# Kernel tuning notes

Hardware: AMD Instinct MI355X
Metric: run time of the kernel (lower is better)

## Reference

```python
import jax, jax.numpy as jnp
import numpy as np

B, N, DIM = 4, 2048, 1024
HEADS, DIM_HEAD = 16, 64
INNER = HEADS * DIM_HEAD


def setup_inputs() -> dict:
    key = jax.random.key(0)
    kx, kw = jax.random.split(key)
    x = jax.random.normal(kx, (B, N, DIM), dtype=jnp.float32)
    # Dense kernel [in_features, out_features], no bias
    w_qkv = jax.random.normal(kw, (DIM, 3 * INNER), dtype=jnp.float32) * (DIM ** -0.5)
    return {"x": x, "w_qkv": w_qkv}


def reference(x, w_qkv):
    scale = DIM_HEAD ** (-0.5)
    qkv = jnp.einsum('bnc,cf->bnf', x, w_qkv)  # [B, N, 3*INNER]
    q, k, v = jnp.split(qkv, 3, axis=-1)
    # 'b n (h d) -> b h n d'
    def to_heads(t):
        return t.reshape(B, N, HEADS, DIM_HEAD).transpose(0, 2, 1, 3)
    q, k, v = map(to_heads, (q, k, v))
    dots = jnp.einsum('bhid,bhjd->bhij', q, k) * scale  # [B, H, N, N]
    attn = jax.nn.softmax(dots, axis=-1)
    out = jnp.einsum('bhij,bhjd->bhid', attn, v)  # [B, H, N, D]
    # 'b h n d -> b n (h d)'
    return out.transpose(0, 2, 1, 3).reshape(B, N, INNER)
```

## Files before the change

kernel.cpp:

```cpp
#include <hip/hip_runtime.h>
#include <hip/hip_bf16.h>
#include <math.h>

typedef __bf16 bf16x2 __attribute__((ext_vector_type(2)));
typedef __bf16 bf16x4 __attribute__((ext_vector_type(4)));
typedef __bf16 bf16x8 __attribute__((ext_vector_type(8)));
typedef float f32x4 __attribute__((ext_vector_type(4)));
typedef float f32x16 __attribute__((ext_vector_type(16)));

#define MFMA16(a, b, c) __builtin_amdgcn_mfma_f32_16x16x32_bf16(a, b, c, 0, 0, 0)
#define MFMA32(a, b, c) __builtin_amdgcn_mfma_f32_32x32x16_bf16(a, b, c, 0, 0, 0)
#define QSCALE 0.1803368801111204f

__device__ __forceinline__ void gload_lds16(const __bf16* g, __bf16* l) {
  __builtin_amdgcn_global_load_lds((const __attribute__((address_space(1))) void*)g,
                                   (__attribute__((address_space(3))) void*)l,
                                   16, 0, 0);
}

__device__ __forceinline__ bf16x2 shflx32(bf16x2 x) {
  int i;
  __builtin_memcpy(&i, &x, 4);
  i = __shfl_xor(i, 32);
  bf16x2 r;
  __builtin_memcpy(&r, &i, 4);
  return r;
}

__global__ __launch_bounds__(256) void convert_x(const float* __restrict__ in,
                                                 __bf16* __restrict__ out) {
  int i = blockIdx.x * 256 + threadIdx.x;
  float4 v = ((const float4*)in)[i];
  bf16x4 o = {(__bf16)v.x, (__bf16)v.y, (__bf16)v.z, (__bf16)v.w};
  *(bf16x4*)&out[i * 4] = o;
}

__global__ __launch_bounds__(256) void transpose_w(const float* __restrict__ W,
                                                   __bf16* __restrict__ Wt) {
  __shared__ __bf16 tile[64][65];
  const int bx = blockIdx.x;
  const int by = blockIdx.y;
  const int t = threadIdx.x;
  const int lr = t >> 6;
  const int lc = t & 63;
  const float sc = (bx < 16) ? QSCALE : 1.0f;
#pragma unroll
  for (int i = 0; i < 16; ++i) {
    int r = lr + i * 4;
    tile[r][lc] = (__bf16)(W[(size_t)(by * 64 + r) * 3072 + bx * 64 + lc] * sc);
  }
  __syncthreads();
#pragma unroll
  for (int i = 0; i < 16; ++i) {
    int r = lr + i * 4;
    Wt[(size_t)(bx * 64 + r) * 1024 + by * 64 + lc] = tile[lc][r];
  }
}

__global__ __launch_bounds__(256) void gemm_qkv(const __bf16* __restrict__ X,
                                                const __bf16* __restrict__ Wt,
                                                __bf16* __restrict__ QKV) {
  __shared__ __bf16 As[128 * 32];
  __shared__ __bf16 Bs[128 * 32];
  const int t = threadIdx.x;
  const int lane = t & 63;
  const int wave = t >> 6;
  const int quad = lane >> 4;
  const int l16 = lane & 15;
  const int n0 = blockIdx.x * 128;
  const int m0 = blockIdx.y * 128;
  const int wm = (wave & 1) * 64;
  const int wn = (wave >> 1) * 64;

  const __bf16* Ag = &X[(size_t)(m0 + wave * 16 + (lane >> 2)) * 1024 + (lane & 3) * 8];
  const __bf16* Bg = &Wt[(size_t)(n0 + wave * 16 + (lane >> 2)) * 1024 + (lane & 3) * 8];
  __bf16* As0 = &As[wave * 512];
  __bf16* As1 = &As[2048 + wave * 512];
  __bf16* Bs0 = &Bs[wave * 512];
  __bf16* Bs1 = &Bs[2048 + wave * 512];

  f32x4 acc[4][4] = {};

  for (int k0 = 0; k0 < 1024; k0 += 32) {
    gload_lds16(Ag + k0, As0);
    gload_lds16(Ag + (size_t)64 * 1024 + k0, As1);
    gload_lds16(Bg + k0, Bs0);
    gload_lds16(Bg + (size_t)64 * 1024 + k0, Bs1);
    __syncthreads();

    bf16x8 af[4], bf[4];
#pragma unroll
    for (int mi = 0; mi < 4; ++mi)
      af[mi] = *(const bf16x8*)&As[(wm + mi * 16 + l16) * 32 + quad * 8];
#pragma unroll
    for (int ni = 0; ni < 4; ++ni)
      bf[ni] = *(const bf16x8*)&Bs[(wn + ni * 16 + l16) * 32 + quad * 8];
#pragma unroll
    for (int mi = 0; mi < 4; ++mi)
#pragma unroll
      for (int ni = 0; ni < 4; ++ni)
        acc[mi][ni] = MFMA16(af[mi], bf[ni], acc[mi][ni]);
    __syncthreads();
  }

#pragma unroll
  for (int mi = 0; mi < 4; ++mi)
#pragma unroll
    for (int ni = 0; ni < 4; ++ni)
#pragma unroll
      for (int r = 0; r < 4; ++r) {
        int row = m0 + wm + mi * 16 + quad * 4 + r;
        int col = n0 + wn + ni * 16 + l16;
        QKV[(size_t)row * 3072 + col] = (__bf16)acc[mi][ni][r];
      }
}

__global__ __launch_bounds__(256) void transpose_v(const __bf16* __restrict__ QKV,
                                                   __bf16* __restrict__ Vt) {
  __shared__ __bf16 tile[64][65];
  const int k0 = blockIdx.x * 64;
  const int h = blockIdx.y;
  const int b = blockIdx.z;
  const int t = threadIdx.x;
  const int lr = t >> 6;
  const int lc = t & 63;
  const __bf16* src = QKV + (size_t)b * 2048 * 3072 + 2048 + h * 64;
  __bf16* dst = Vt + (size_t)(b * 16 + h) * 64 * 2048;
#pragma unroll
  for (int i = 0; i < 16; ++i) {
    int r = lr + i * 4;
    tile[r][lc] = src[(size_t)(k0 + r) * 3072 + lc];
  }
  __syncthreads();
#pragma unroll
  for (int i = 0; i < 16; ++i) {
    int d = lr + i * 4;
    dst[(size_t)d * 2048 + k0 + lc] = tile[lc][d];
  }
}

#define AT_LD 72

__global__ __launch_bounds__(256) void attn(const __bf16* __restrict__ QKV,
                                            const __bf16* __restrict__ Vt,
                                            float* __restrict__ Out) {
  const int h = blockIdx.y;
  const int b = blockIdx.z;
  const int t = threadIdx.x;
  const int lane = t & 63;
  const int wave = t >> 6;
  const int l31 = lane & 31;
  const int half = lane >> 5;
  const int q0w = blockIdx.x * 128 + wave * 32;

  const size_t base = (size_t)b * 2048 * 3072;
  const __bf16* Qb = QKV + base + h * 64;
  const __bf16* Kb = QKV + base + 1024 + h * 64;
  const __bf16* Vtb = Vt + (size_t)(b * 16 + h) * 64 * 2048;

  __shared__ __bf16 Ks[64 * AT_LD];
  __shared__ __bf16 Vs[64 * AT_LD];

  bf16x8 qf[4];
#pragma unroll
  for (int dc = 0; dc < 4; ++dc)
    qf[dc] = *(const bf16x8*)&Qb[(size_t)(q0w + l31) * 3072 + dc * 16 + half * 8];

  f32x16 o[2] = {};
  float lsum = 0.0f;

  const int srow = t >> 2;
  const int sc = (t & 3) * 16;

  for (int kv0 = 0; kv0 < 2048; kv0 += 64) {
    bf16x8 k0v = *(const bf16x8*)&Kb[(size_t)(kv0 + srow) * 3072 + sc];
    bf16x8 k1v = *(const bf16x8*)&Kb[(size_t)(kv0 + srow) * 3072 + sc + 8];
    bf16x8 v0v = *(const bf16x8*)&Vtb[(size_t)srow * 2048 + kv0 + sc];
    bf16x8 v1v = *(const bf16x8*)&Vtb[(size_t)srow * 2048 + kv0 + sc + 8];
    __syncthreads();
    *(bf16x8*)&Ks[srow * AT_LD + sc] = k0v;
    *(bf16x8*)&Ks[srow * AT_LD + sc + 8] = k1v;
    *(bf16x8*)&Vs[srow * AT_LD + sc] = v0v;
    *(bf16x8*)&Vs[srow * AT_LD + sc + 8] = v1v;
    __syncthreads();

    bf16x2 pp[2][4][2];
#pragma unroll
    for (int kt = 0; kt < 2; ++kt) {
      f32x16 c = {};
#pragma unroll
      for (int dc = 0; dc < 4; ++dc) {
        bf16x8 kf = *(const bf16x8*)&Ks[(kt * 32 + l31) * AT_LD + dc * 16 + half * 8];
        c = MFMA32(kf, qf[dc], c);
      }
#pragma unroll
      for (int g = 0; g < 4; ++g)
#pragma unroll
        for (int p = 0; p < 2; ++p) {
          float e0 = __builtin_amdgcn_exp2f(c[g * 4 + p * 2]);
          float e1 = __builtin_amdgcn_exp2f(c[g * 4 + p * 2 + 1]);
          lsum += e0 + e1;
          pp[kt][g][p] = bf16x2{(__bf16)e0, (__bf16)e1};
        }
    }

    bf16x8 pf[4];
#pragma unroll
    for (int kk = 0; kk < 4; ++kk) {
      const int kt = kk >> 1;
      const int g0 = (2 * kk) & 3;
      const int g1 = (2 * kk + 1) & 3;
      bf16x2 x0 = pp[kt][g0][0], x1 = pp[kt][g0][1];
      bf16x2 y0 = pp[kt][g1][0], y1 = pp[kt][g1][1];
      bf16x2 a0 = half ? y0 : x0;
      bf16x2 a1 = half ? y1 : x1;
      bf16x2 r0 = shflx32(half ? x0 : y0);
      bf16x2 r1 = shflx32(half ? x1 : y1);
      union { bf16x8 v; bf16x2 hh[4]; } f;
      f.hh[0] = half ? r0 : a0;
      f.hh[1] = half ? r1 : a1;
      f.hh[2] = half ? a0 : r0;
      f.hh[3] = half ? a1 : r1;
      pf[kk] = f.v;
    }

#pragma unroll
    for (int dt = 0; dt < 2; ++dt)
#pragma unroll
      for (int kk = 0; kk < 4; ++kk) {
        bf16x8 vf = *(const bf16x8*)&Vs[(dt * 32 + l31) * AT_LD + kk * 16 + half * 8];
        o[dt] = MFMA32(pf[kk], vf, o[dt]);
      }
  }

  lsum += __shfl_xor(lsum, 32);
  float inv = 1.0f / lsum;

  float iv[16];
#pragma unroll
  for (int r = 0; r < 16; ++r)
    iv[r] = __shfl(inv, (r & 3) + 8 * (r >> 2) + 4 * half);

#pragma unroll
  for (int dt = 0; dt < 2; ++dt)
#pragma unroll
    for (int r = 0; r < 16; ++r) {
      int qr = (r & 3) + 8 * (r >> 2) + 4 * half;
      Out[(size_t)(b * 2048 + q0w + qr) * 1024 + h * 64 + dt * 32 + l31] =
          o[dt][r] * iv[r];
    }
}

extern "C" void kernel_launch(void* const* d_in, const int* in_sizes, int n_in,
                              void* d_out, int out_size, void* d_ws, size_t ws_size,
                              hipStream_t stream) {
  const float* x = (const float*)d_in[0];
  const float* w = (const float*)d_in[1];
  float* out = (float*)d_out;

  __bf16* Wt = (__bf16*)d_ws;
  __bf16* QKV = Wt + (size_t)3072 * 1024;
  __bf16* Xb = QKV + (size_t)8192 * 3072;
  __bf16* Vtr = Xb;

  convert_x<<<8192, 256, 0, stream>>>(x, Xb);
  transpose_w<<<dim3(48, 16), 256, 0, stream>>>(w, Wt);
  gemm_qkv<<<dim3(24, 64), 256, 0, stream>>>(Xb, Wt, QKV);
  transpose_v<<<dim3(32, 16, 4), 256, 0, stream>>>(QKV, Vtr);
  attn<<<dim3(16, 16, 4), 256, 0, stream>>>(QKV, Vtr, out);
}
```

Baseline: 263.5 us.

## Fuse V transpose into QKV GEMM epilogue and drop cross-lane P shuffles

The QKV GEMM epilogue now writes Q and K into a 2048-wide buffer and writes V directly in transposed per-head layout, which removes the separate transpose_v kernel and its extra global round trip. In attention, K rows are stored into shared memory with a permuted row index, so the MFMA score output already lands in the register order the PV MFMA expects. That lets the exp results pack straight into bf16x8 operands without the xor-32 shuffles and selects. The V stores in the epilogue are 8-byte, strided writes that may coalesce poorly.

```diff
diff --git a/kernel.cpp b/kernel.cpp
--- a/kernel.cpp
+++ b/kernel.cpp
@@ -16,15 +16,6 @@
   __builtin_amdgcn_global_load_lds((const __attribute__((address_space(1))) void*)g,
                                    (__attribute__((address_space(3))) void*)l,
                                    16, 0, 0);
-}
-
-__device__ __forceinline__ bf16x2 shflx32(bf16x2 x) {
-  int i;
-  __builtin_memcpy(&i, &x, 4);
-  i = __shfl_xor(i, 32);
-  bf16x2 r;
-  __builtin_memcpy(&r, &i, 4);
-  return r;
 }
 
 __global__ __launch_bounds__(256) void convert_x(const float* __restrict__ in,
@@ -59,7 +50,8 @@
 
 __global__ __launch_bounds__(256) void gemm_qkv(const __bf16* __restrict__ X,
                                                 const __bf16* __restrict__ Wt,
-                                                __bf16* __restrict__ QKV) {
+                                                __bf16* __restrict__ QK,
+                                                __bf16* __restrict__ Vt) {
   __shared__ __bf16 As[128 * 32];
   __shared__ __bf16 Bs[128 * 32];
   const int t = threadIdx.x;
@@ -103,45 +95,36 @@
     __syncthreads();
   }
 
-#pragma unroll
-  for (int mi = 0; mi < 4; ++mi)
-#pragma unroll
-    for (int ni = 0; ni < 4; ++ni)
-#pragma unroll
-      for (int r = 0; r < 4; ++r) {
-        int row = m0 + wm + mi * 16 + quad * 4 + r;
-        int col = n0 + wn + ni * 16 + l16;
-        QKV[(size_t)row * 3072 + col] = (__bf16)acc[mi][ni][r];
-      }
-}
-
-__global__ __launch_bounds__(256) void transpose_v(const __bf16* __restrict__ QKV,
-                                                   __bf16* __restrict__ Vt) {
-  __shared__ __bf16 tile[64][65];
-  const int k0 = blockIdx.x * 64;
-  const int h = blockIdx.y;
-  const int b = blockIdx.z;
-  const int t = threadIdx.x;
-  const int lr = t >> 6;
-  const int lc = t & 63;
-  const __bf16* src = QKV + (size_t)b * 2048 * 3072 + 2048 + h * 64;
-  __bf16* dst = Vt + (size_t)(b * 16 + h) * 64 * 2048;
-#pragma unroll
-  for (int i = 0; i < 16; ++i) {
-    int r = lr + i * 4;
-    tile[r][lc] = src[(size_t)(k0 + r) * 3072 + lc];
-  }
-  __syncthreads();
-#pragma unroll
-  for (int i = 0; i < 16; ++i) {
-    int d = lr + i * 4;
-    dst[(size_t)d * 2048 + k0 + lc] = tile[lc][d];
+  if (n0 < 2048) {
+#pragma unroll
+    for (int mi = 0; mi < 4; ++mi)
+#pragma unroll
+      for (int ni = 0; ni < 4; ++ni)
+#pragma unroll
+        for (int r = 0; r < 4; ++r) {
+          int row = m0 + wm + mi * 16 + quad * 4 + r;
+          int col = n0 + wn + ni * 16 + l16;
+          QK[(size_t)row * 2048 + col] = (__bf16)acc[mi][ni][r];
+        }
+  } else {
+#pragma unroll
+    for (int mi = 0; mi < 4; ++mi)
+#pragma unroll
+      for (int ni = 0; ni < 4; ++ni) {
+        int v = n0 + wn + ni * 16 + l16 - 2048;
+        int hh = v >> 6, d = v & 63;
+        int row0 = m0 + wm + mi * 16 + quad * 4;
+        int bb = row0 >> 11, key = row0 & 2047;
+        bf16x4 pk = {(__bf16)acc[mi][ni][0], (__bf16)acc[mi][ni][1],
+                     (__bf16)acc[mi][ni][2], (__bf16)acc[mi][ni][3]};
+        *(bf16x4*)&Vt[((size_t)(bb * 16 + hh) * 64 + d) * 2048 + key] = pk;
+      }
   }
 }
 
 #define AT_LD 72
 
-__global__ __launch_bounds__(256) void attn(const __bf16* __restrict__ QKV,
+__global__ __launch_bounds__(256) void attn(const __bf16* __restrict__ QK,
                                             const __bf16* __restrict__ Vt,
                                             float* __restrict__ Out) {
   const int h = blockIdx.y;
@@ -153,9 +136,9 @@
   const int half = lane >> 5;
   const int q0w = blockIdx.x * 128 + wave * 32;
 
-  const size_t base = (size_t)b * 2048 * 3072;
-  const __bf16* Qb = QKV + base + h * 64;
-  const __bf16* Kb = QKV + base + 1024 + h * 64;
+  const size_t base = (size_t)b * 2048 * 2048;
+  const __bf16* Qb = QK + base + h * 64;
+  const __bf16* Kb = QK + base + 1024 + h * 64;
   const __bf16* Vtb = Vt + (size_t)(b * 16 + h) * 64 * 2048;
 
   __shared__ __bf16 Ks[64 * AT_LD];
@@ -164,27 +147,28 @@
   bf16x8 qf[4];
 #pragma unroll
   for (int dc = 0; dc < 4; ++dc)
-    qf[dc] = *(const bf16x8*)&Qb[(size_t)(q0w + l31) * 3072 + dc * 16 + half * 8];
+    qf[dc] = *(const bf16x8*)&Qb[(size_t)(q0w + l31) * 2048 + dc * 16 + half * 8];
 
   f32x16 o[2] = {};
   float lsum = 0.0f;
 
   const int srow = t >> 2;
   const int sc = (t & 3) * 16;
+  const int prow = (srow & 51) | ((srow & 4) << 1) | ((srow & 8) >> 1);
 
   for (int kv0 = 0; kv0 < 2048; kv0 += 64) {
-    bf16x8 k0v = *(const bf16x8*)&Kb[(size_t)(kv0 + srow) * 3072 + sc];
-    bf16x8 k1v = *(const bf16x8*)&Kb[(size_t)(kv0 + srow) * 3072 + sc + 8];
+    bf16x8 k0v = *(const bf16x8*)&Kb[(size_t)(kv0 + srow) * 2048 + sc];
+    bf16x8 k1v = *(const bf16x8*)&Kb[(size_t)(kv0 + srow) * 2048 + sc + 8];
     bf16x8 v0v = *(const bf16x8*)&Vtb[(size_t)srow * 2048 + kv0 + sc];
     bf16x8 v1v = *(const bf16x8*)&Vtb[(size_t)srow * 2048 + kv0 + sc + 8];
     __syncthreads();
-    *(bf16x8*)&Ks[srow * AT_LD + sc] = k0v;
-    *(bf16x8*)&Ks[srow * AT_LD + sc + 8] = k1v;
+    *(bf16x8*)&Ks[prow * AT_LD + sc] = k0v;
+    *(bf16x8*)&Ks[prow * AT_LD + sc + 8] = k1v;
     *(bf16x8*)&Vs[srow * AT_LD + sc] = v0v;
     *(bf16x8*)&Vs[srow * AT_LD + sc + 8] = v1v;
     __syncthreads();
 
-    bf16x2 pp[2][4][2];
+    bf16x8 pf[4];
 #pragma unroll
     for (int kt = 0; kt < 2; ++kt) {
       f32x16 c = {};
@@ -194,34 +178,16 @@
         c = MFMA32(kf, qf[dc], c);
       }
 #pragma unroll
-      for (int g = 0; g < 4; ++g)
-#pragma unroll
-        for (int p = 0; p < 2; ++p) {
-          float e0 = __builtin_amdgcn_exp2f(c[g * 4 + p * 2]);
-          float e1 = __builtin_amdgcn_exp2f(c[g * 4 + p * 2 + 1]);
-          lsum += e0 + e1;
-          pp[kt][g][p] = bf16x2{(__bf16)e0, (__bf16)e1};
+      for (int kkl = 0; kkl < 2; ++kkl) {
+        bf16x8 f;
+#pragma unroll
+        for (int j = 0; j < 8; ++j) {
+          float e = __builtin_amdgcn_exp2f(c[8 * kkl + 4 * (j >> 2) + (j & 3)]);
+          lsum += e;
+          f[j] = (__bf16)e;
         }
-    }
-
-    bf16x8 pf[4];
-#pragma unroll
-    for (int kk = 0; kk < 4; ++kk) {
-      const int kt = kk >> 1;
-      const int g0 = (2 * kk) & 3;
-      const int g1 = (2 * kk + 1) & 3;
-      bf16x2 x0 = pp[kt][g0][0], x1 = pp[kt][g0][1];
-      bf16x2 y0 = pp[kt][g1][0], y1 = pp[kt][g1][1];
-      bf16x2 a0 = half ? y0 : x0;
-      bf16x2 a1 = half ? y1 : x1;
-      bf16x2 r0 = shflx32(half ? x0 : y0);
-      bf16x2 r1 = shflx32(half ? x1 : y1);
-      union { bf16x8 v; bf16x2 hh[4]; } f;
-      f.hh[0] = half ? r0 : a0;
-      f.hh[1] = half ? r1 : a1;
-      f.hh[2] = half ? a0 : r0;
-      f.hh[3] = half ? a1 : r1;
-      pf[kk] = f.v;
+        pf[kt * 2 + kkl] = f;
+      }
     }
 
 #pragma unroll
@@ -259,13 +225,12 @@
   float* out = (float*)d_out;
 
   __bf16* Wt = (__bf16*)d_ws;
-  __bf16* QKV = Wt + (size_t)3072 * 1024;
-  __bf16* Xb = QKV + (size_t)8192 * 3072;
-  __bf16* Vtr = Xb;
+  __bf16* QK = Wt + (size_t)3072 * 1024;
+  __bf16* Xb = QK + (size_t)8192 * 2048;
+  __bf16* Vtr = Xb + (size_t)8192 * 1024;
 
   convert_x<<<8192, 256, 0, stream>>>(x, Xb);
   transpose_w<<<dim3(48, 16), 256, 0, stream>>>(w, Wt);
-  gemm_qkv<<<dim3(24, 64), 256, 0, stream>>>(Xb, Wt, QKV);
-  transpose_v<<<dim3(32, 16, 4), 256, 0, stream>>>(QKV, Vtr);
-  attn<<<dim3(16, 16, 4), 256, 0, stream>>>(QKV, Vtr, out);
-}
+  gemm_qkv<<<dim3(24, 64), 256, 0, stream>>>(Xb, Wt, QK, Vtr);
+  attn<<<dim3(16, 16, 4), 256, 0, stream>>>(QK, Vtr, out);
+}
```

After: 234.3 us. 11.0% less time.
